# Kernel tuning notes

Hardware: AMD Instinct MI355X
Metric: run time of the kernel (lower is better)

The kernel has to match this reference:

```python
import jax, jax.numpy as jnp
import numpy as np

B, S, D, L = 4, 4096, 2048, 4
QH, KVH, WINDOW = 16, 4, 512
HD = D // QH
G = QH // KVH
CAPF = 0.25
EPS = float(jnp.finfo(jnp.float32).eps)  # torch RMSNorm default eps for fp32


def setup_inputs() -> dict:
    key = jax.random.key(0)
    ks = jax.random.split(key, 8)
    s = 0.02
    return {
        "x": jax.random.normal(ks[0], (B, S, D), jnp.float32),
        "router_w": jax.random.normal(ks[1], (1, D), jnp.float32) * s,
        "norm1_w": jnp.ones((L, D), jnp.float32),
        "norm2_w": jnp.ones((L, D), jnp.float32),
        "qkv_w": jax.random.normal(ks[2], (L, (QH + 2 * KVH) * HD, D), jnp.float32) * s,
        "proj_w": jax.random.normal(ks[3], (L, D, D), jnp.float32) * s,
        "fc1_w": jax.random.normal(ks[4], (L, 2 * D, D), jnp.float32) * s,
        "fc2_w": jax.random.normal(ks[5], (L, D, D), jnp.float32) * s,
    }


def rmsnorm(x, w):
    return x * jax.lax.rsqrt(jnp.mean(x * x, -1, keepdims=True) + EPS) * w


def gqa(x, qkv_w, proj_w):
    # x: [B, C, D]; causal sliding-window attention with ALiBi (flash_attn semantics)
    b, c, _ = x.shape
    qkv = x @ qkv_w.T
    q = qkv[..., : QH * HD].reshape(b, c, KVH, G, HD)
    k = qkv[..., QH * HD:(QH + KVH) * HD].reshape(b, c, KVH, HD)
    v = qkv[..., (QH + KVH) * HD:].reshape(b, c, KVH, HD)
    scale = 1.0 / np.sqrt(HD)
    scores = jnp.einsum('bqkgd,bskd->bkgqs', q, k) * scale  # [B,KVH,G,C,C]
    i = jnp.arange(c)[:, None]
    j = jnp.arange(c)[None, :]
    diff = (i - j).astype(jnp.float32)
    mask = (diff >= 0) & (diff <= WINDOW)  # causal + left window
    slopes = jnp.exp2(-((jnp.arange(QH, dtype=jnp.float32) + 1.0) * 8.0 / QH))
    slopes = slopes.reshape(KVH, G, 1, 1)  # q head h = kvh*G + g ordering
    scores = jnp.where(mask, scores - slopes * diff, -jnp.inf)
    p = jax.nn.softmax(scores, axis=-1)
    att = jnp.einsum('bkgqs,bskd->bqkgd', p, v).reshape(b, c, QH * HD)
    return att @ proj_w.T


def swiglu(x, fc1_w, fc2_w):
    h = x @ fc1_w.T
    a, gate = jnp.split(h, 2, axis=-1)
    return (jax.nn.silu(gate) * a) @ fc2_w.T


def reference(x, router_w, norm1_w, norm2_w, qkv_w, proj_w, fc1_w, fc2_w):
    b, s, d = x.shape
    rw = jax.nn.sigmoid(x @ router_w.T)  # [B, S, 1]
    cap = int(s * CAPF)  # training path: capacity = int(seq_len * capacity_factor)
    rws = rw[..., 0]
    _, top_idx = jax.lax.top_k(rws, cap)            # unsorted-by-position top-k
    idx_sorted = jnp.sort(top_idx, axis=1)          # restore sequence order
    order = jnp.argsort(top_idx, axis=1)
    # faithful to source: gathers router_weights at the sort-order permutation
    # indices (values in [0, cap)), exactly as torch.gather(router_weights, 1, router_top_order)
    top_w = jnp.take_along_axis(rws, order, axis=1)[..., None]  # [B, cap, 1]
    lat = jnp.take_along_axis(x, idx_sorted[..., None], axis=1)  # [B, cap, D]
    for l in range(L):
        lat = lat + gqa(rmsnorm(lat, norm1_w[l]), qkv_w[l], proj_w[l])
        lat = lat + swiglu(rmsnorm(lat, norm2_w[l]), fc1_w[l], fc2_w[l])
    lat = lat * top_w
    bidx = jnp.arange(b)[:, None]
    pred = jnp.zeros_like(x).at[bidx, idx_sorted].set(lat)
    decisions = jnp.zeros_like(rw).at[bidx, idx_sorted].set(1.0)
    return pred, rw, decisions
```

## Files before the change

### kernel.cpp

```cpp
#include <hip/hip_runtime.h>
#include <hip/hip_bf16.h>

constexpr int NB = 4;
constexpr int SEQ = 4096;
constexpr int DIM = 2048;
constexpr int NLAYER = 4;
constexpr int NQH = 16;
constexpr int NKVH = 4;
constexpr int WIN = 512;
constexpr int HDIM = 128;
constexpr int CAPN = 1024;
constexpr int MTOK = NB * CAPN;
constexpr int QKVN = (NQH + 2 * NKVH) * HDIM;
constexpr int VOFF = DIM + NKVH * HDIM;
constexpr float EPSF = 1.1920928955078125e-07f;

typedef __hip_bfloat16 bf16;
typedef __bf16 b16x8 __attribute__((ext_vector_type(8)));
typedef __bf16 b16x4 __attribute__((ext_vector_type(4)));
typedef float f32x4 __attribute__((ext_vector_type(4)));

#define MFMA16(a, b, c) __builtin_amdgcn_mfma_f32_16x16x32_bf16((a), (b), (c), 0, 0, 0)

__device__ __forceinline__ void gload_lds16(const void* g, void* l) {
  __builtin_amdgcn_global_load_lds((__attribute__((address_space(1))) void*)(void*)g,
                                   (__attribute__((address_space(3))) void*)l, 16, 0, 0);
}

__global__ __launch_bounds__(256) void cast_kernel(const float* __restrict__ in,
                                                   bf16* __restrict__ out, int n) {
  int i = (blockIdx.x * 256 + threadIdx.x) * 4;
  if (i >= n) return;
  float4 v = *(const float4*)(in + i);
  b16x4 o;
  o[0] = (__bf16)v.x; o[1] = (__bf16)v.y; o[2] = (__bf16)v.z; o[3] = (__bf16)v.w;
  *(b16x4*)((__bf16*)out + i) = o;
}

__global__ __launch_bounds__(256) void router_kernel(const float* __restrict__ x,
                                                     const float* __restrict__ rwt,
                                                     float* __restrict__ rw_out) {
  int tok = blockIdx.x * 4 + (threadIdx.x >> 6);
  int l = threadIdx.x & 63;
  const float* xr = x + (size_t)tok * DIM;
  float s = 0.f;
  for (int c = l; c < DIM; c += 64) s += xr[c] * rwt[c];
  for (int off = 32; off; off >>= 1) s += __shfl_down(s, off);
  if (l == 0) rw_out[tok] = 1.f / (1.f + expf(-s));
}

__global__ __launch_bounds__(256) void rankcnt_kernel(const float* __restrict__ rw,
                                                      int* __restrict__ rank) {
  int blk = blockIdx.x;
  int ic = blk & 15, jc = (blk >> 4) & 15, b = blk >> 8;
  __shared__ float4 svi[64];
  int t = threadIdx.x;
  if (t < 64) svi[t] = ((const float4*)(rw + (size_t)b * SEQ + ic * 256))[t];
  __syncthreads();
  int j = jc * 256 + t;
  float vj = rw[(size_t)b * SEQ + j];
  int r = 0;
#pragma unroll 16
  for (int q = 0; q < 64; ++q) {
    float4 v = svi[q];
    int i = ic * 256 + q * 4;
    r += (v.x > vj || (v.x == vj && (i + 0) < j)) ? 1 : 0;
    r += (v.y > vj || (v.y == vj && (i + 1) < j)) ? 1 : 0;
    r += (v.z > vj || (v.z == vj && (i + 2) < j)) ? 1 : 0;
    r += (v.w > vj || (v.w == vj && (i + 3) < j)) ? 1 : 0;
  }
  atomicAdd(&rank[b * SEQ + j], r);
}

__global__ __launch_bounds__(1024) void select_kernel(const int* __restrict__ rank,
                                                      const float* __restrict__ rw,
                                                      int* __restrict__ idxs,
                                                      float* __restrict__ topw,
                                                      float* __restrict__ dec) {
  int b = blockIdx.x;
  int t = threadIdx.x;
  __shared__ int sr[SEQ];
  __shared__ int scnt[1024];
  for (int i = t; i < SEQ; i += 1024) sr[i] = rank[b * SEQ + i];
  __syncthreads();
  for (int i = t; i < SEQ; i += 1024) dec[(size_t)b * SEQ + i] = (sr[i] < CAPN) ? 1.0f : 0.0f;
  int c = 0;
#pragma unroll
  for (int k = 0; k < 4; ++k) c += (sr[t * 4 + k] < CAPN) ? 1 : 0;
  scnt[t] = c;
  __syncthreads();
  for (int off = 1; off < 1024; off <<= 1) {
    int v = scnt[t];
    int vm = (t >= off) ? scnt[t - off] : 0;
    __syncthreads();
    scnt[t] = v + vm;
    __syncthreads();
  }
  int pos = scnt[t] - c;
  for (int k = 0; k < 4; ++k) {
    int j = t * 4 + k;
    int r = sr[j];
    if (r < CAPN) {
      idxs[b * CAPN + pos] = j;
      topw[b * CAPN + pos] = rw[(size_t)b * SEQ + r];
      pos++;
    }
  }
}

__global__ __launch_bounds__(256) void gather_kernel(const float* __restrict__ x,
                                                     const int* __restrict__ idxs,
                                                     float* __restrict__ lat) {
  int tok = blockIdx.x;
  int b = tok >> 10, i = tok & 1023;
  int src = idxs[b * CAPN + i];
  const float4* sp = (const float4*)(x + ((size_t)b * SEQ + src) * DIM);
  float4* dp = (float4*)(lat + (size_t)tok * DIM);
  int t = threadIdx.x;
  dp[t] = sp[t];
  dp[t + 256] = sp[t + 256];
}

__global__ __launch_bounds__(256) void rmsnorm_kernel(const float* __restrict__ in,
                                                      const float* __restrict__ w,
                                                      bf16* __restrict__ out) {
  int row = blockIdx.x;
  int t = threadIdx.x;
  const float4* sp = (const float4*)(in + (size_t)row * DIM);
  float4 v0 = sp[t], v1 = sp[t + 256];
  float ss = v0.x * v0.x + v0.y * v0.y + v0.z * v0.z + v0.w * v0.w +
             v1.x * v1.x + v1.y * v1.y + v1.z * v1.z + v1.w * v1.w;
  for (int off = 32; off; off >>= 1) ss += __shfl_down(ss, off);
  __shared__ float red[4];
  if ((t & 63) == 0) red[t >> 6] = ss;
  __syncthreads();
  float total = red[0] + red[1] + red[2] + red[3];
  float sc = rsqrtf(total * (1.0f / DIM) + EPSF);
  const float4* wp = (const float4*)w;
  float4 w0 = wp[t], w1 = wp[t + 256];
  __bf16* op = (__bf16*)out + (size_t)row * DIM;
  b16x4 o0, o1;
  o0[0] = (__bf16)(v0.x * w0.x * sc); o0[1] = (__bf16)(v0.y * w0.y * sc);
  o0[2] = (__bf16)(v0.z * w0.z * sc); o0[3] = (__bf16)(v0.w * w0.w * sc);
  o1[0] = (__bf16)(v1.x * w1.x * sc); o1[1] = (__bf16)(v1.y * w1.y * sc);
  o1[2] = (__bf16)(v1.z * w1.z * sc); o1[3] = (__bf16)(v1.w * w1.w * sc);
  *(b16x4*)(op + t * 4) = o0;
  *(b16x4*)(op + 1024 + t * 4) = o1;
}


template <int ROWS>
__device__ __forceinline__ void stage_tile(const bf16* gbase, int ldk, int kt,
                                           bf16* lbuf, int tid) {
#pragma unroll
  for (int i = 0; i < ROWS / 128; ++i) {
    int q = i * 8192 + tid * 16;
    int row = q >> 6;
    int ce = ((tid & 3) ^ ((row >> 1) & 3)) << 3;
    gload_lds16((const __bf16*)gbase + (size_t)row * ldk + kt * 32 + ce,
                (char*)lbuf + q);
  }
}

__device__ __forceinline__ b16x8 frag_ld(const bf16* buf, int row, int hi) {
  int ce = (hi ^ ((row >> 1) & 3)) << 3;
  return *(const b16x8*)((const __bf16*)buf + row * 32 + ce);
}

template <int MR, bool ADD, bool OUTBF>
__global__ __launch_bounds__(512, 2) void gemm256(const bf16* __restrict__ A,
                                                  const bf16* __restrict__ Bw,
                                                  float* __restrict__ Cf,
                                                  bf16* __restrict__ Cb,
                                                  bf16* __restrict__ vTout,
                                                  int N, int K, int nbn) {
  constexpr int BM = MR * 32;
  constexpr int PH = MR / 4;
  __shared__ __align__(16) bf16 sA[4][BM * 32];
  __shared__ __align__(16) bf16 sB[4][256 * 32];
  const int tid = threadIdx.x;
  const int w = tid >> 6, l = tid & 63;
  const int lo = l & 15, hi = l >> 4;
  const int wm = w >> 2, wn = w & 3;
  const int nwg = gridDim.x;
  int bid = blockIdx.x;
  bid = (bid & 7) * (nwg >> 3) + (bid >> 3);
  const int bm = bid / nbn, bn = bid % nbn;
  const bf16* Ab = A + (size_t)bm * BM * K;
  const bf16* Bb = Bw + (size_t)bn * 256 * K;
  const int nt = K >> 5;

  f32x4 acc[MR][4];
#pragma unroll
  for (int i = 0; i < MR; ++i)
#pragma unroll
    for (int j = 0; j < 4; ++j) acc[i][j] = f32x4{0.f, 0.f, 0.f, 0.f};

  for (int tt = 0; tt < 3; ++tt) {
    stage_tile<BM>(Ab, K, tt, sA[tt], tid);
    stage_tile<256>(Bb, K, tt, sB[tt], tid);
  }
  if constexpr (MR == 8) asm volatile("s_waitcnt vmcnt(8)" ::: "memory");
  else                   asm volatile("s_waitcnt vmcnt(6)" ::: "memory");
  __builtin_amdgcn_sched_barrier(0);
  __builtin_amdgcn_s_barrier();

  for (int t = 0; t < nt; ++t) {
    const bf16* bufA = sA[t & 3];
    const bf16* bufB = sB[t & 3];
    b16x8 bfr[4];
#pragma unroll
    for (int p = 0; p < PH; ++p) {
      b16x8 af[4];
#pragma unroll
      for (int mi = 0; mi < 4; ++mi)
        af[mi] = frag_ld(bufA, wm * (MR * 16) + p * 64 + mi * 16 + lo, hi);
      if (p == 0) {
#pragma unroll
        for (int ni = 0; ni < 4; ++ni)
          bfr[ni] = frag_ld(bufB, wn * 64 + ni * 16 + lo, hi);
      }
      if (t + 3 < nt) {
        if (p == 0) stage_tile<BM>(Ab, K, t + 3, sA[(t + 3) & 3], tid);
        if (p == PH - 1) stage_tile<256>(Bb, K, t + 3, sB[(t + 3) & 3], tid);
      }
      __builtin_amdgcn_s_barrier();
      __builtin_amdgcn_s_setprio(1);
#pragma unroll
      for (int mi = 0; mi < 4; ++mi)
#pragma unroll
        for (int ni = 0; ni < 4; ++ni)
          acc[p * 4 + mi][ni] = MFMA16(af[mi], bfr[ni], acc[p * 4 + mi][ni]);
      __builtin_amdgcn_s_setprio(0);
      if (p == PH - 1) {
        if (t + 3 < nt) {
          if constexpr (MR == 8) asm volatile("s_waitcnt vmcnt(8)" ::: "memory");
          else                   asm volatile("s_waitcnt vmcnt(6)" ::: "memory");
        } else if (t + 2 < nt) {
          if constexpr (MR == 8) asm volatile("s_waitcnt vmcnt(4)" ::: "memory");
          else                   asm volatile("s_waitcnt vmcnt(3)" ::: "memory");
        } else if (t + 1 < nt) {
          asm volatile("s_waitcnt vmcnt(0)" ::: "memory");
        }
        __builtin_amdgcn_sched_barrier(0);
      }
      __builtin_amdgcn_s_barrier();
    }
  }

#pragma unroll
  for (int mi = 0; mi < MR; ++mi) {
    int row0 = bm * BM + wm * (MR * 16) + mi * 16 + hi * 4;
#pragma unroll
    for (int ni = 0; ni < 4; ++ni) {
      int col = bn * 256 + wn * 64 + ni * 16 + lo;
#pragma unroll
      for (int r = 0; r < 4; ++r) {
        size_t idx = (size_t)(row0 + r) * N + col;
        float v = acc[mi][ni][r];
        if constexpr (ADD) v += Cf[idx];
        if constexpr (OUTBF) {
          bf16 bv = __float2bfloat16(v);
          Cb[idx] = bv;
          if (vTout != nullptr && col >= VOFF) {
            int cc = col - VOFF;
            int kvh = cc >> 7, d = cc & 127;
            int row = row0 + r;
            int bb = row >> 10, tk = row & 1023;
            vTout[((size_t)(bb * NKVH + kvh) * HDIM + d) * CAPN + tk] = bv;
          }
        } else {
          Cf[idx] = v;
        }
      }
    }
  }
}

__global__ __launch_bounds__(256) void attn_kernel(const bf16* __restrict__ qkvb,
                                                   const bf16* __restrict__ vT,
                                                   bf16* __restrict__ attb) {
  const int blk = blockIdx.x;
  const int qc = blk & 31;
  const int kvh = (blk >> 5) & 3;
  const int b = blk >> 7;
  const int w = threadIdx.x >> 6, l = threadIdx.x & 63;
  const int lo = l & 15, hi = l >> 4;
  const int h = kvh * 4 + w;
  const float slope = exp2f(-0.5f * (float)(h + 1));
  const float scale = 0.08838834764831845f;
  __shared__ __align__(16) bf16 p_lds[4][2][16 * 32];
  const __bf16* qp = (const __bf16*)qkvb;
  const __bf16* vtp = (const __bf16*)vT + (size_t)(b * NKVH + kvh) * HDIM * CAPN;
  const size_t tb = (size_t)b * CAPN;
  const int i0b = qc * 32;

  b16x8 aq[2][4];
#pragma unroll
  for (int qt = 0; qt < 2; ++qt) {
    const __bf16* qrow = qp + (tb + i0b + qt * 16 + lo) * QKVN + h * HDIM + hi * 8;
#pragma unroll
    for (int c = 0; c < 4; ++c) aq[qt][c] = *(const b16x8*)(qrow + c * 32);
  }

  f32x4 acc[2][8];
#pragma unroll
  for (int qt = 0; qt < 2; ++qt)
#pragma unroll
    for (int d = 0; d < 8; ++d) acc[qt][d] = f32x4{0.f, 0.f, 0.f, 0.f};
  float mrow[2][4], ssum[2][4];
#pragma unroll
  for (int qt = 0; qt < 2; ++qt)
#pragma unroll
    for (int r = 0; r < 4; ++r) { mrow[qt][r] = -1e30f; ssum[qt][r] = 0.f; }

  int jlo = i0b - WIN;
  if (jlo < 0) jlo = 0;
  jlo &= ~31;
  for (int j0 = jlo; j0 <= i0b; j0 += 32) {
    b16x8 kf[2][4];
#pragma unroll
    for (int jt = 0; jt < 2; ++jt) {
      const __bf16* krow = qp + (tb + j0 + jt * 16 + lo) * QKVN + DIM + kvh * HDIM + hi * 8;
#pragma unroll
      for (int c = 0; c < 4; ++c) kf[jt][c] = *(const b16x8*)(krow + c * 32);
    }
    f32x4 s[2][2];
#pragma unroll
    for (int qt = 0; qt < 2; ++qt)
#pragma unroll
      for (int jt = 0; jt < 2; ++jt) {
        s[qt][jt] = f32x4{0.f, 0.f, 0.f, 0.f};
#pragma unroll
        for (int c = 0; c < 4; ++c) s[qt][jt] = MFMA16(aq[qt][c], kf[jt][c], s[qt][jt]);
      }
#pragma unroll
    for (int qt = 0; qt < 2; ++qt) {
#pragma unroll
      for (int r = 0; r < 4; ++r) {
        const int i = i0b + qt * 16 + hi * 4 + r;
        float d0f = (float)(i - (j0 + lo));
        float d1f = (float)(i - (j0 + 16 + lo));
        float v0 = (d0f >= 0.f && d0f <= 512.f) ? (s[qt][0][r] * scale - slope * d0f) : -1e30f;
        float v1 = (d1f >= 0.f && d1f <= 512.f) ? (s[qt][1][r] * scale - slope * d1f) : -1e30f;
        float tm = fmaxf(v0, v1);
#pragma unroll
        for (int off = 1; off < 16; off <<= 1) tm = fmaxf(tm, __shfl_xor(tm, off));
        float mnew = fmaxf(mrow[qt][r], tm);
        float e0 = (v0 > -1e29f) ? __expf(v0 - mnew) : 0.f;
        float e1 = (v1 > -1e29f) ? __expf(v1 - mnew) : 0.f;
        float rs = e0 + e1;
#pragma unroll
        for (int off = 1; off < 16; off <<= 1) rs += __shfl_xor(rs, off);
        float corr = (mrow[qt][r] > -1e29f) ? __expf(mrow[qt][r] - mnew) : 0.f;
        ssum[qt][r] = ssum[qt][r] * corr + rs;
        mrow[qt][r] = mnew;
#pragma unroll
        for (int d = 0; d < 8; ++d) acc[qt][d][r] *= corr;
        p_lds[w][qt][(hi * 4 + r) * 32 + lo] = __float2bfloat16(e0);
        p_lds[w][qt][(hi * 4 + r) * 32 + 16 + lo] = __float2bfloat16(e1);
      }
    }
    b16x8 pa[2];
    pa[0] = *(const b16x8*)((const __bf16*)p_lds[w][0] + lo * 32 + hi * 8);
    pa[1] = *(const b16x8*)((const __bf16*)p_lds[w][1] + lo * 32 + hi * 8);
#pragma unroll
    for (int dh = 0; dh < 2; ++dh) {
      b16x8 bv[4];
#pragma unroll
      for (int dd = 0; dd < 4; ++dd) {
        int d = dh * 4 + dd;
        bv[dd] = *(const b16x8*)(vtp + (size_t)(d * 16 + lo) * CAPN + j0 + hi * 8);
      }
#pragma unroll
      for (int qt = 0; qt < 2; ++qt)
#pragma unroll
        for (int dd = 0; dd < 4; ++dd)
          acc[qt][dh * 4 + dd] = MFMA16(pa[qt], bv[dd], acc[qt][dh * 4 + dd]);
    }
  }
#pragma unroll
  for (int qt = 0; qt < 2; ++qt)
#pragma unroll
    for (int d = 0; d < 8; ++d)
#pragma unroll
      for (int r = 0; r < 4; ++r) {
        int row = i0b + qt * 16 + hi * 4 + r;
        attb[(tb + row) * DIM + h * HDIM + d * 16 + lo] =
            __float2bfloat16(acc[qt][d][r] / ssum[qt][r]);
      }
}

__global__ __launch_bounds__(256) void swiglu_kernel(const bf16* __restrict__ hb,
                                                     bf16* __restrict__ out) {
  int row = blockIdx.x;
  int c = threadIdx.x * 8;
  const __bf16* hp = (const __bf16*)hb + (size_t)row * (2 * DIM);
  b16x8 a8 = *(const b16x8*)(hp + c);
  b16x8 g8 = *(const b16x8*)(hp + DIM + c);
  b16x8 o;
#pragma unroll
  for (int i = 0; i < 8; ++i) {
    float a = (float)a8[i], g = (float)g8[i];
    float sg = g / (1.f + __expf(-g));
    o[i] = (__bf16)(sg * a);
  }
  *(b16x8*)((__bf16*)out + (size_t)row * DIM + c) = o;
}

__global__ __launch_bounds__(256) void scatter_kernel(const float* __restrict__ lat,
                                                      const int* __restrict__ idxs,
                                                      const float* __restrict__ topw,
                                                      float* __restrict__ pred) {
  int tok = blockIdx.x;
  int b = tok >> 10, i = tok & 1023;
  int dst = idxs[b * CAPN + i];
  float wv = topw[b * CAPN + i];
  const float4* sp = (const float4*)(lat + (size_t)tok * DIM);
  float4* dp = (float4*)(pred + ((size_t)b * SEQ + dst) * DIM);
  int t = threadIdx.x;
  float4 v = sp[t];
  v.x *= wv; v.y *= wv; v.z *= wv; v.w *= wv;
  dp[t] = v;
  v = sp[t + 256];
  v.x *= wv; v.y *= wv; v.z *= wv; v.w *= wv;
  dp[t + 256] = v;
}

extern "C" void kernel_launch(void* const* d_in, const int* in_sizes, int n_in,
                              void* d_out, int out_size, void* d_ws, size_t ws_size,
                              hipStream_t stream) {
  const float* x        = (const float*)d_in[0];
  const float* router_w = (const float*)d_in[1];
  const float* norm1_w  = (const float*)d_in[2];
  const float* norm2_w  = (const float*)d_in[3];
  const float* qkv_w    = (const float*)d_in[4];
  const float* proj_w   = (const float*)d_in[5];
  const float* fc1_w    = (const float*)d_in[6];
  const float* fc2_w    = (const float*)d_in[7];

  float* pred   = (float*)d_out;
  float* rw_out = pred + (size_t)NB * SEQ * DIM;
  float* dec    = rw_out + (size_t)NB * SEQ;

  char* ws = (char*)d_ws;
  float* lat  = (float*)ws; ws += (size_t)MTOK * DIM * 4;
  bf16* xn    = (bf16*)ws;  ws += (size_t)MTOK * DIM * 2;
  bf16* qkvb  = (bf16*)ws;  ws += (size_t)MTOK * QKVN * 2;
  bf16* attb  = (bf16*)ws;  ws += (size_t)MTOK * DIM * 2;
  int* rank   = (int*)ws;   ws += (size_t)NB * SEQ * 4;
  int* idxs   = (int*)ws;   ws += (size_t)NB * CAPN * 4;
  float* topw = (float*)ws; ws += (size_t)NB * CAPN * 4;

  char* sp = (char*)pred;
  bf16* hb = (bf16*)sp; sp += (size_t)MTOK * (2 * DIM) * 2;
  bf16* wq = (bf16*)sp; sp += (size_t)QKVN * DIM * 2;
  bf16* wp = (bf16*)sp; sp += (size_t)DIM * DIM * 2;
  bf16* w1 = (bf16*)sp; sp += (size_t)(2 * DIM) * DIM * 2;
  bf16* w2 = (bf16*)sp; sp += (size_t)DIM * DIM * 2;
  bf16* vT = (bf16*)sp; sp += (size_t)NB * NKVH * HDIM * CAPN * 2;

  router_kernel<<<NB * SEQ / 4, 256, 0, stream>>>(x, router_w, rw_out);
  hipMemsetAsync(rank, 0, (size_t)NB * SEQ * 4, stream);
  rankcnt_kernel<<<NB * 256, 256, 0, stream>>>(rw_out, rank);
  select_kernel<<<NB, 1024, 0, stream>>>(rank, rw_out, idxs, topw, dec);
  gather_kernel<<<MTOK, 256, 0, stream>>>(x, idxs, lat);

  for (int l = 0; l < NLAYER; ++l) {
    cast_kernel<<<(QKVN * DIM) / 1024, 256, 0, stream>>>(qkv_w + (size_t)l * QKVN * DIM, wq, QKVN * DIM);
    cast_kernel<<<(DIM * DIM) / 1024, 256, 0, stream>>>(proj_w + (size_t)l * DIM * DIM, wp, DIM * DIM);
    cast_kernel<<<(2 * DIM * DIM) / 1024, 256, 0, stream>>>(fc1_w + (size_t)l * 2 * DIM * DIM, w1, 2 * DIM * DIM);
    cast_kernel<<<(DIM * DIM) / 1024, 256, 0, stream>>>(fc2_w + (size_t)l * DIM * DIM, w2, DIM * DIM);

    rmsnorm_kernel<<<MTOK, 256, 0, stream>>>(lat, norm1_w + (size_t)l * DIM, xn);
    gemm256<8, false, true><<<(MTOK / 256) * (QKVN / 256), 512, 0, stream>>>(
        xn, wq, nullptr, qkvb, vT, QKVN, DIM, QKVN / 256);
    attn_kernel<<<NB * NKVH * 32, 256, 0, stream>>>(qkvb, vT, attb);
    gemm256<4, true, false><<<(MTOK / 128) * (DIM / 256), 512, 0, stream>>>(
        attb, wp, lat, nullptr, nullptr, DIM, DIM, DIM / 256);

    rmsnorm_kernel<<<MTOK, 256, 0, stream>>>(lat, norm2_w + (size_t)l * DIM, xn);
    gemm256<8, false, true><<<(MTOK / 256) * (2 * DIM / 256), 512, 0, stream>>>(
        xn, w1, nullptr, hb, nullptr, 2 * DIM, DIM, 2 * DIM / 256);
    swiglu_kernel<<<MTOK, 256, 0, stream>>>(hb, xn);
    gemm256<4, true, false><<<(MTOK / 128) * (DIM / 256), 512, 0, stream>>>(
        xn, w2, lat, nullptr, nullptr, DIM, DIM, DIM / 256);
  }

  hipMemsetAsync(pred, 0, (size_t)NB * SEQ * DIM * 4, stream);
  scatter_kernel<<<MTOK, 256, 0, stream>>>(lat, idxs, topw, pred);
}
```

Before: 1.704 ms.

## Add 8-wave ping-pong GEMM with BK=64 tiles for QKV and FC1 projections

Introduces a new 256x256 GEMM kernel that uses 64-wide K tiles with XOR-swizzled LDS, double buffering, and a fine-grained schedule interleaving half-tile global loads with quadrant MFMA blocks separated by barriers and priority hints. It also remaps block IDs across eight groups to improve L2 locality. The QKV and FC1 GEMMs switch to it, and the old kernel drops its V-transpose epilogue. The aim is better overlap of memory loads with MFMA work. The cost is a larger LDS footprint (128 KB) and many barriers, which could hurt occupancy or add stalls.

Result: no change. 1.675 ms (-1.7%).

```diff
diff --git a/kernel.cpp b/kernel.cpp
--- a/kernel.cpp
+++ b/kernel.cpp
@@ -149,6 +149,150 @@
 }
 
 
+__device__ __forceinline__ void stage_half(const bf16* g, int K, int kt,
+                                           bf16* tilebase, int h, int tid) {
+#pragma unroll
+  for (int j = 0; j < 2; ++j) {
+    int q = h * 16384 + j * 8192 + tid * 16;
+    int row = q >> 7;
+    int sc = ((tid & 7) ^ (row & 7)) << 3;
+    gload_lds16((const __bf16*)g + (size_t)row * K + kt * 64 + sc,
+                (char*)tilebase + q);
+  }
+}
+
+__device__ __forceinline__ b16x8 frag8(const bf16* buf, int row, int ks, int hi) {
+  int co = (ks * 32 + hi * 8) ^ ((row & 7) << 3);
+  return *(const b16x8*)((const __bf16*)buf + row * 64 + co);
+}
+
+template <bool VT>
+__global__ __launch_bounds__(512) void gemm8p(const bf16* __restrict__ A,
+                                              const bf16* __restrict__ Bw,
+                                              bf16* __restrict__ Cb,
+                                              bf16* __restrict__ vTout,
+                                              int N, int K, int nbn) {
+  __shared__ __align__(16) bf16 sA[2][256 * 64];
+  __shared__ __align__(16) bf16 sB[2][256 * 64];
+  const int tid = threadIdx.x;
+  const int w = tid >> 6, l = tid & 63;
+  const int lo = l & 15, hi = l >> 4;
+  const int wm = w >> 2, wn = w & 3;
+  const int nwg = gridDim.x;
+  int bid = blockIdx.x;
+  bid = (bid & 7) * (nwg >> 3) + (bid >> 3);
+  const int bm = bid / nbn, bn = bid % nbn;
+  const bf16* Ab = A + (size_t)bm * 256 * K;
+  const bf16* Bb = Bw + (size_t)bn * 256 * K;
+  const int nt = K >> 6;
+  const int niter = nt >> 1;
+
+  f32x4 acc[8][4];
+#pragma unroll
+  for (int i = 0; i < 8; ++i)
+#pragma unroll
+    for (int j = 0; j < 4; ++j) acc[i][j] = f32x4{0.f, 0.f, 0.f, 0.f};
+
+#define LDA_Q(BUF, QM)                                                      \
+  do {                                                                      \
+    _Pragma("unroll") for (int mi = 0; mi < 4; ++mi)                        \
+        _Pragma("unroll") for (int ks = 0; ks < 2; ++ks)                    \
+            af[mi][ks] = frag8((BUF), wm * 128 + (QM)*64 + mi * 16 + lo, ks, hi); \
+  } while (0)
+#define LDB_Q(BUF, QN, DST)                                                 \
+  do {                                                                      \
+    _Pragma("unroll") for (int ni = 0; ni < 2; ++ni)                        \
+        _Pragma("unroll") for (int ks = 0; ks < 2; ++ks)                    \
+            DST[ni][ks] = frag8((BUF), wn * 64 + (QN)*32 + ni * 16 + lo, ks, hi); \
+  } while (0)
+#define MM_Q(QM, QN, BFR)                                                   \
+  do {                                                                      \
+    __builtin_amdgcn_s_setprio(1);                                          \
+    _Pragma("unroll") for (int ks = 0; ks < 2; ++ks)                        \
+        _Pragma("unroll") for (int mi = 0; mi < 4; ++mi)                    \
+            _Pragma("unroll") for (int ni = 0; ni < 2; ++ni)                \
+                acc[(QM)*4 + mi][(QN)*2 + ni] =                             \
+                    MFMA16(af[mi][ks], BFR[ni][ks], acc[(QM)*4 + mi][(QN)*2 + ni]); \
+    __builtin_amdgcn_s_setprio(0);                                          \
+  } while (0)
+#define BAR() __builtin_amdgcn_s_barrier()
+
+  stage_half(Ab, K, 0, sA[0], 0, tid);
+  stage_half(Ab, K, 0, sA[0], 1, tid);
+  stage_half(Bb, K, 0, sB[0], 0, tid);
+  stage_half(Bb, K, 0, sB[0], 1, tid);
+  stage_half(Bb, K, 1, sB[1], 0, tid);
+  stage_half(Bb, K, 1, sB[1], 1, tid);
+  stage_half(Ab, K, 1, sA[1], 0, tid);
+  asm volatile("s_waitcnt vmcnt(6)" ::: "memory");
+  __builtin_amdgcn_sched_barrier(0);
+  BAR();
+
+  for (int i = 0; i < niter; ++i) {
+    const int t0 = 2 * i;
+    const bool s2 = (t0 + 2) < nt;
+    b16x8 af[4][2], bf0[2][2], bf1[2][2];
+    LDA_Q(sA[0], 0); LDB_Q(sB[0], 0, bf0);
+    stage_half(Ab, K, t0 + 1, sA[1], 1, tid);
+    BAR(); MM_Q(0, 0, bf0); BAR();
+    LDB_Q(sB[0], 1, bf1);
+    BAR(); MM_Q(0, 1, bf1); BAR();
+    LDA_Q(sA[0], 1);
+    if (s2) stage_half(Bb, K, t0 + 2, sB[0], 0, tid);
+    BAR(); MM_Q(1, 0, bf0); BAR();
+    if (s2) stage_half(Bb, K, t0 + 2, sB[0], 1, tid);
+    BAR(); MM_Q(1, 1, bf1);
+    if (s2) asm volatile("s_waitcnt vmcnt(4)" ::: "memory");
+    else    asm volatile("s_waitcnt vmcnt(0)" ::: "memory");
+    __builtin_amdgcn_sched_barrier(0);
+    BAR();
+    LDA_Q(sA[1], 0); LDB_Q(sB[1], 0, bf0);
+    if (s2) stage_half(Ab, K, t0 + 2, sA[0], 0, tid);
+    BAR(); MM_Q(0, 0, bf0); BAR();
+    LDB_Q(sB[1], 1, bf1);
+    if (s2) stage_half(Ab, K, t0 + 2, sA[0], 1, tid);
+    BAR(); MM_Q(0, 1, bf1); BAR();
+    LDA_Q(sA[1], 1);
+    if (s2) { stage_half(Bb, K, t0 + 3, sB[1], 0, tid);
+              stage_half(Bb, K, t0 + 3, sB[1], 1, tid); }
+    BAR(); MM_Q(1, 0, bf0); BAR();
+    if (s2) stage_half(Ab, K, t0 + 3, sA[1], 0, tid);
+    BAR(); MM_Q(1, 1, bf1);
+    if (s2) {
+      asm volatile("s_waitcnt vmcnt(6)" ::: "memory");
+      __builtin_amdgcn_sched_barrier(0);
+    }
+    BAR();
+  }
+#undef LDA_Q
+#undef LDB_Q
+#undef MM_Q
+#undef BAR
+
+#pragma unroll
+  for (int fi = 0; fi < 8; ++fi) {
+    int row0 = bm * 256 + wm * 128 + fi * 16 + hi * 4;
+#pragma unroll
+    for (int fj = 0; fj < 4; ++fj) {
+      int col = bn * 256 + wn * 64 + fj * 16 + lo;
+#pragma unroll
+      for (int r = 0; r < 4; ++r) {
+        bf16 bv = __float2bfloat16(acc[fi][fj][r]);
+        Cb[(size_t)(row0 + r) * N + col] = bv;
+        if constexpr (VT) {
+          if (col >= VOFF) {
+            int cc = col - VOFF;
+            int kvh = cc >> 7, d = cc & 127;
+            int row = row0 + r;
+            int bb = row >> 10, tk = row & 1023;
+            vTout[((size_t)(bb * NKVH + kvh) * HDIM + d) * CAPN + tk] = bv;
+          }
+        }
+      }
+    }
+  }
+}
+
 template <int ROWS>
 __device__ __forceinline__ void stage_tile(const bf16* gbase, int ldk, int kt,
                                            bf16* lbuf, int tid) {
@@ -260,15 +404,7 @@
         float v = acc[mi][ni][r];
         if constexpr (ADD) v += Cf[idx];
         if constexpr (OUTBF) {
-          bf16 bv = __float2bfloat16(v);
-          Cb[idx] = bv;
-          if (vTout != nullptr && col >= VOFF) {
-            int cc = col - VOFF;
-            int kvh = cc >> 7, d = cc & 127;
-            int row = row0 + r;
-            int bb = row >> 10, tk = row & 1023;
-            vTout[((size_t)(bb * NKVH + kvh) * HDIM + d) * CAPN + tk] = bv;
-          }
+          Cb[idx] = __float2bfloat16(v);
         } else {
           Cf[idx] = v;
         }
@@ -473,15 +609,15 @@
     cast_kernel<<<(DIM * DIM) / 1024, 256, 0, stream>>>(fc2_w + (size_t)l * DIM * DIM, w2, DIM * DIM);
 
     rmsnorm_kernel<<<MTOK, 256, 0, stream>>>(lat, norm1_w + (size_t)l * DIM, xn);
-    gemm256<8, false, true><<<(MTOK / 256) * (QKVN / 256), 512, 0, stream>>>(
-        xn, wq, nullptr, qkvb, vT, QKVN, DIM, QKVN / 256);
+    gemm8p<true><<<(MTOK / 256) * (QKVN / 256), 512, 0, stream>>>(
+        xn, wq, qkvb, vT, QKVN, DIM, QKVN / 256);
     attn_kernel<<<NB * NKVH * 32, 256, 0, stream>>>(qkvb, vT, attb);
     gemm256<4, true, false><<<(MTOK / 128) * (DIM / 256), 512, 0, stream>>>(
         attb, wp, lat, nullptr, nullptr, DIM, DIM, DIM / 256);
 
     rmsnorm_kernel<<<MTOK, 256, 0, stream>>>(lat, norm2_w + (size_t)l * DIM, xn);
-    gemm256<8, false, true><<<(MTOK / 256) * (2 * DIM / 256), 512, 0, stream>>>(
-        xn, w1, nullptr, hb, nullptr, 2 * DIM, DIM, 2 * DIM / 256);
+    gemm8p<false><<<(MTOK / 256) * (2 * DIM / 256), 512, 0, stream>>>(
+        xn, w1, hb, nullptr, 2 * DIM, DIM, 2 * DIM / 256);
     swiglu_kernel<<<MTOK, 256, 0, stream>>>(hb, xn);
     gemm256<4, true, false><<<(MTOK / 128) * (DIM / 256), 512, 0, stream>>>(
         xn, w2, lat, nullptr, nullptr, DIM, DIM, DIM / 256);
```

## Replace pipelined GEMM with simpler 128x128 kernel and fuse SwiGLU into fc1

Applied to the files above, without the earlier changes.

Swaps the 256-wide, 4-stage software-pipelined GEMM for a 128x128 tile GEMM with a single LDS buffer, a BK of 64 and synchronous staging at 256 threads per block. The fc1 weight rows are interleaved in 16-row chunks of value and gate during the cast, so each output tile holds matching value and gate columns and SwiGLU is applied in the GEMM epilogue. This removes the separate swiglu kernel and the round trip of the 2*DIM hidden buffer. The trade-off is losing multi-stage prefetch and overlap of loads with MFMA, which may expose memory latency.

After: 1.499 ms. 1.14x faster.

```diff
diff --git a/kernel.cpp b/kernel.cpp
--- a/kernel.cpp
+++ b/kernel.cpp
@@ -37,6 +37,23 @@
   *(b16x4*)((__bf16*)out + i) = o;
 }
 
+__global__ __launch_bounds__(256) void cast_fc1_kernel(const float* __restrict__ in,
+                                                       bf16* __restrict__ out) {
+  int p = blockIdx.x;
+  int chunk = p >> 5, w = p & 31;
+  int L = (w < 16) ? (chunk * 16 + w) : (DIM + chunk * 16 + (w - 16));
+  const float4* spv = (const float4*)(in + (size_t)L * DIM);
+  __bf16* op = (__bf16*)out + (size_t)p * DIM;
+  int t = threadIdx.x;
+#pragma unroll
+  for (int j = 0; j < 2; ++j) {
+    float4 v = spv[t + j * 256];
+    b16x4 o;
+    o[0] = (__bf16)v.x; o[1] = (__bf16)v.y; o[2] = (__bf16)v.z; o[3] = (__bf16)v.w;
+    *(b16x4*)(op + (t + j * 256) * 4) = o;
+  }
+}
+
 __global__ __launch_bounds__(256) void router_kernel(const float* __restrict__ x,
                                                      const float* __restrict__ rwt,
                                                      float* __restrict__ rw_out) {
@@ -114,11 +131,11 @@
   int tok = blockIdx.x;
   int b = tok >> 10, i = tok & 1023;
   int src = idxs[b * CAPN + i];
-  const float4* sp = (const float4*)(x + ((size_t)b * SEQ + src) * DIM);
+  const float4* spv = (const float4*)(x + ((size_t)b * SEQ + src) * DIM);
   float4* dp = (float4*)(lat + (size_t)tok * DIM);
   int t = threadIdx.x;
-  dp[t] = sp[t];
-  dp[t + 256] = sp[t + 256];
+  dp[t] = spv[t];
+  dp[t + 256] = spv[t + 256];
 }
 
 __global__ __launch_bounds__(256) void rmsnorm_kernel(const float* __restrict__ in,
@@ -126,8 +143,8 @@
                                                       bf16* __restrict__ out) {
   int row = blockIdx.x;
   int t = threadIdx.x;
-  const float4* sp = (const float4*)(in + (size_t)row * DIM);
-  float4 v0 = sp[t], v1 = sp[t + 256];
+  const float4* spv = (const float4*)(in + (size_t)row * DIM);
+  float4 v0 = spv[t], v1 = spv[t + 256];
   float ss = v0.x * v0.x + v0.y * v0.y + v0.z * v0.z + v0.w * v0.w +
              v1.x * v1.x + v1.y * v1.y + v1.z * v1.z + v1.w * v1.w;
   for (int off = 32; off; off >>= 1) ss += __shfl_down(ss, off);
@@ -149,128 +166,110 @@
 }
 
 
-template <int ROWS>
-__device__ __forceinline__ void stage_tile(const bf16* gbase, int ldk, int kt,
-                                           bf16* lbuf, int tid) {
-#pragma unroll
-  for (int i = 0; i < ROWS / 128; ++i) {
-    int q = i * 8192 + tid * 16;
-    int row = q >> 6;
-    int ce = ((tid & 3) ^ ((row >> 1) & 3)) << 3;
-    gload_lds16((const __bf16*)gbase + (size_t)row * ldk + kt * 32 + ce,
-                (char*)lbuf + q);
-  }
-}
-
-__device__ __forceinline__ b16x8 frag_ld(const bf16* buf, int row, int hi) {
-  int ce = (hi ^ ((row >> 1) & 3)) << 3;
-  return *(const b16x8*)((const __bf16*)buf + row * 32 + ce);
-}
-
-template <int MR, bool ADD, bool OUTBF>
-__global__ __launch_bounds__(512, 2) void gemm256(const bf16* __restrict__ A,
-                                                  const bf16* __restrict__ Bw,
-                                                  float* __restrict__ Cf,
-                                                  bf16* __restrict__ Cb,
-                                                  bf16* __restrict__ vTout,
-                                                  int N, int K, int nbn) {
-  constexpr int BM = MR * 32;
-  constexpr int PH = MR / 4;
-  __shared__ __align__(16) bf16 sA[4][BM * 32];
-  __shared__ __align__(16) bf16 sB[4][256 * 32];
+__device__ __forceinline__ void stage97(const bf16* g, int K, int kt,
+                                        bf16* tile, int tid) {
+#pragma unroll
+  for (int j = 0; j < 4; ++j) {
+    int q = j * 4096 + tid * 16;
+    int row = q >> 7;
+    int sc = ((tid & 7) ^ (row & 7)) << 3;
+    gload_lds16((const __bf16*)g + (size_t)row * K + kt * 64 + sc,
+                (char*)tile + q);
+  }
+}
+
+__device__ __forceinline__ b16x8 frag97(const bf16* buf, int row, int ks, int hi) {
+  int co = (ks * 32 + hi * 8) ^ ((row & 7) << 3);
+  return *(const b16x8*)((const __bf16*)buf + row * 64 + co);
+}
+
+template <int MODE>
+__global__ __launch_bounds__(256, 3) void gemm97(const bf16* __restrict__ A,
+                                                 const bf16* __restrict__ Bw,
+                                                 float* __restrict__ Cf,
+                                                 bf16* __restrict__ Cb,
+                                                 bf16* __restrict__ vTout,
+                                                 int N, int K, int nbn) {
+  __shared__ __align__(16) bf16 sA[128 * 64];
+  __shared__ __align__(16) bf16 sB[128 * 64];
   const int tid = threadIdx.x;
   const int w = tid >> 6, l = tid & 63;
   const int lo = l & 15, hi = l >> 4;
-  const int wm = w >> 2, wn = w & 3;
+  const int wr = w >> 1, wc = w & 1;
   const int nwg = gridDim.x;
   int bid = blockIdx.x;
   bid = (bid & 7) * (nwg >> 3) + (bid >> 3);
   const int bm = bid / nbn, bn = bid % nbn;
-  const bf16* Ab = A + (size_t)bm * BM * K;
-  const bf16* Bb = Bw + (size_t)bn * 256 * K;
-  const int nt = K >> 5;
-
-  f32x4 acc[MR][4];
-#pragma unroll
-  for (int i = 0; i < MR; ++i)
+  const bf16* Ab = A + (size_t)bm * 128 * K;
+  const bf16* Bb = Bw + (size_t)bn * 128 * K;
+  const int nt = K >> 6;
+
+  f32x4 acc[4][4];
+#pragma unroll
+  for (int i = 0; i < 4; ++i)
 #pragma unroll
     for (int j = 0; j < 4; ++j) acc[i][j] = f32x4{0.f, 0.f, 0.f, 0.f};
 
-  for (int tt = 0; tt < 3; ++tt) {
-    stage_tile<BM>(Ab, K, tt, sA[tt], tid);
-    stage_tile<256>(Bb, K, tt, sB[tt], tid);
-  }
-  if constexpr (MR == 8) asm volatile("s_waitcnt vmcnt(8)" ::: "memory");
-  else                   asm volatile("s_waitcnt vmcnt(6)" ::: "memory");
-  __builtin_amdgcn_sched_barrier(0);
-  __builtin_amdgcn_s_barrier();
-
   for (int t = 0; t < nt; ++t) {
-    const bf16* bufA = sA[t & 3];
-    const bf16* bufB = sB[t & 3];
-    b16x8 bfr[4];
-#pragma unroll
-    for (int p = 0; p < PH; ++p) {
-      b16x8 af[4];
+    stage97(Ab, K, t, sA, tid);
+    stage97(Bb, K, t, sB, tid);
+    __syncthreads();
+#pragma unroll
+    for (int ks = 0; ks < 2; ++ks) {
+      b16x8 af[4], bfm[4];
 #pragma unroll
       for (int mi = 0; mi < 4; ++mi)
-        af[mi] = frag_ld(bufA, wm * (MR * 16) + p * 64 + mi * 16 + lo, hi);
-      if (p == 0) {
+        af[mi] = frag97(sA, wr * 64 + mi * 16 + lo, ks, hi);
+#pragma unroll
+      for (int ni = 0; ni < 4; ++ni)
+        bfm[ni] = frag97(sB, wc * 64 + ni * 16 + lo, ks, hi);
+#pragma unroll
+      for (int mi = 0; mi < 4; ++mi)
 #pragma unroll
         for (int ni = 0; ni < 4; ++ni)
-          bfr[ni] = frag_ld(bufB, wn * 64 + ni * 16 + lo, hi);
-      }
-      if (t + 3 < nt) {
-        if (p == 0) stage_tile<BM>(Ab, K, t + 3, sA[(t + 3) & 3], tid);
-        if (p == PH - 1) stage_tile<256>(Bb, K, t + 3, sB[(t + 3) & 3], tid);
-      }
-      __builtin_amdgcn_s_barrier();
-      __builtin_amdgcn_s_setprio(1);
-#pragma unroll
-      for (int mi = 0; mi < 4; ++mi)
-#pragma unroll
-        for (int ni = 0; ni < 4; ++ni)
-          acc[p * 4 + mi][ni] = MFMA16(af[mi], bfr[ni], acc[p * 4 + mi][ni]);
-      __builtin_amdgcn_s_setprio(0);
-      if (p == PH - 1) {
-        if (t + 3 < nt) {
-          if constexpr (MR == 8) asm volatile("s_waitcnt vmcnt(8)" ::: "memory");
-          else                   asm volatile("s_waitcnt vmcnt(6)" ::: "memory");
-        } else if (t + 2 < nt) {
-          if constexpr (MR == 8) asm volatile("s_waitcnt vmcnt(4)" ::: "memory");
-          else                   asm volatile("s_waitcnt vmcnt(3)" ::: "memory");
-        } else if (t + 1 < nt) {
-          asm volatile("s_waitcnt vmcnt(0)" ::: "memory");
+          acc[mi][ni] = MFMA16(af[mi], bfm[ni], acc[mi][ni]);
+    }
+    __syncthreads();
+  }
+
+#pragma unroll
+  for (int mi = 0; mi < 4; ++mi) {
+    int row0 = bm * 128 + wr * 64 + mi * 16 + hi * 4;
+    if constexpr (MODE == 2) {
+#pragma unroll
+      for (int j2 = 0; j2 < 2; ++j2) {
+        int colL = bn * 64 + wc * 32 + j2 * 16 + lo;
+#pragma unroll
+        for (int r = 0; r < 4; ++r) {
+          float a = acc[mi][2 * j2][r];
+          float g = acc[mi][2 * j2 + 1][r];
+          float s = g / (1.f + __expf(-g));
+          Cb[(size_t)(row0 + r) * DIM + colL] = __float2bfloat16(a * s);
         }
-        __builtin_amdgcn_sched_barrier(0);
-      }
-      __builtin_amdgcn_s_barrier();
-    }
-  }
-
-#pragma unroll
-  for (int mi = 0; mi < MR; ++mi) {
-    int row0 = bm * BM + wm * (MR * 16) + mi * 16 + hi * 4;
-#pragma unroll
-    for (int ni = 0; ni < 4; ++ni) {
-      int col = bn * 256 + wn * 64 + ni * 16 + lo;
-#pragma unroll
-      for (int r = 0; r < 4; ++r) {
-        size_t idx = (size_t)(row0 + r) * N + col;
-        float v = acc[mi][ni][r];
-        if constexpr (ADD) v += Cf[idx];
-        if constexpr (OUTBF) {
-          bf16 bv = __float2bfloat16(v);
-          Cb[idx] = bv;
-          if (vTout != nullptr && col >= VOFF) {
-            int cc = col - VOFF;
-            int kvh = cc >> 7, d = cc & 127;
-            int row = row0 + r;
-            int bb = row >> 10, tk = row & 1023;
-            vTout[((size_t)(bb * NKVH + kvh) * HDIM + d) * CAPN + tk] = bv;
+      }
+    } else {
+#pragma unroll
+      for (int ni = 0; ni < 4; ++ni) {
+        int col = bn * 128 + wc * 64 + ni * 16 + lo;
+#pragma unroll
+        for (int r = 0; r < 4; ++r) {
+          size_t idx = (size_t)(row0 + r) * N + col;
+          float v = acc[mi][ni][r];
+          if constexpr (MODE == 3) {
+            Cf[idx] += v;
+          } else {
+            bf16 bv = __float2bfloat16(v);
+            Cb[idx] = bv;
+            if constexpr (MODE == 1) {
+              if (col >= VOFF) {
+                int cc = col - VOFF;
+                int kvh = cc >> 7, d = cc & 127;
+                int row = row0 + r;
+                int bb = row >> 10, tk = row & 1023;
+                vTout[((size_t)(bb * NKVH + kvh) * HDIM + d) * CAPN + tk] = bv;
+              }
+            }
           }
-        } else {
-          Cf[idx] = v;
         }
       }
     }
@@ -391,23 +390,6 @@
       }
 }
 
-__global__ __launch_bounds__(256) void swiglu_kernel(const bf16* __restrict__ hb,
-                                                     bf16* __restrict__ out) {
-  int row = blockIdx.x;
-  int c = threadIdx.x * 8;
-  const __bf16* hp = (const __bf16*)hb + (size_t)row * (2 * DIM);
-  b16x8 a8 = *(const b16x8*)(hp + c);
-  b16x8 g8 = *(const b16x8*)(hp + DIM + c);
-  b16x8 o;
-#pragma unroll
-  for (int i = 0; i < 8; ++i) {
-    float a = (float)a8[i], g = (float)g8[i];
-    float sg = g / (1.f + __expf(-g));
-    o[i] = (__bf16)(sg * a);
-  }
-  *(b16x8*)((__bf16*)out + (size_t)row * DIM + c) = o;
-}
-
 __global__ __launch_bounds__(256) void scatter_kernel(const float* __restrict__ lat,
                                                       const int* __restrict__ idxs,
                                                       const float* __restrict__ topw,
@@ -416,13 +398,13 @@
   int b = tok >> 10, i = tok & 1023;
   int dst = idxs[b * CAPN + i];
   float wv = topw[b * CAPN + i];
-  const float4* sp = (const float4*)(lat + (size_t)tok * DIM);
+  const float4* spv = (const float4*)(lat + (size_t)tok * DIM);
   float4* dp = (float4*)(pred + ((size_t)b * SEQ + dst) * DIM);
   int t = threadIdx.x;
-  float4 v = sp[t];
+  float4 v = spv[t];
   v.x *= wv; v.y *= wv; v.z *= wv; v.w *= wv;
   dp[t] = v;
-  v = sp[t + 256];
+  v = spv[t + 256];
   v.x *= wv; v.y *= wv; v.z *= wv; v.w *= wv;
   dp[t + 256] = v;
 }
@@ -453,7 +435,7 @@
   float* topw = (float*)ws; ws += (size_t)NB * CAPN * 4;
 
   char* sp = (char*)pred;
-  bf16* hb = (bf16*)sp; sp += (size_t)MTOK * (2 * DIM) * 2;
+  sp += (size_t)MTOK * (2 * DIM) * 2;
   bf16* wq = (bf16*)sp; sp += (size_t)QKVN * DIM * 2;
   bf16* wp = (bf16*)sp; sp += (size_t)DIM * DIM * 2;
   bf16* w1 = (bf16*)sp; sp += (size_t)(2 * DIM) * DIM * 2;
@@ -469,22 +451,21 @@
   for (int l = 0; l < NLAYER; ++l) {
     cast_kernel<<<(QKVN * DIM) / 1024, 256, 0, stream>>>(qkv_w + (size_t)l * QKVN * DIM, wq, QKVN * DIM);
     cast_kernel<<<(DIM * DIM) / 1024, 256, 0, stream>>>(proj_w + (size_t)l * DIM * DIM, wp, DIM * DIM);
-    cast_kernel<<<(2 * DIM * DIM) / 1024, 256, 0, stream>>>(fc1_w + (size_t)l * 2 * DIM * DIM, w1, 2 * DIM * DIM);
+    cast_fc1_kernel<<<2 * DIM, 256, 0, stream>>>(fc1_w + (size_t)l * 2 * DIM * DIM, w1);
     cast_kernel<<<(DIM * DIM) / 1024, 256, 0, stream>>>(fc2_w + (size_t)l * DIM * DIM, w2, DIM * DIM);
 
     rmsnorm_kernel<<<MTOK, 256, 0, stream>>>(lat, norm1_w + (size_t)l * DIM, xn);
-    gemm256<8, false, true><<<(MTOK / 256) * (QKVN / 256), 512, 0, stream>>>(
-        xn, wq, nullptr, qkvb, vT, QKVN, DIM, QKVN / 256);
+    gemm97<1><<<(MTOK / 128) * (QKVN / 128), 256, 0, stream>>>(
+        xn, wq, nullptr, qkvb, vT, QKVN, DIM, QKVN / 128);
     attn_kernel<<<NB * NKVH * 32, 256, 0, stream>>>(qkvb, vT, attb);
-    gemm256<4, true, false><<<(MTOK / 128) * (DIM / 256), 512, 0, stream>>>(
-        attb, wp, lat, nullptr, nullptr, DIM, DIM, DIM / 256);
+    gemm97<3><<<(MTOK / 128) * (DIM / 128), 256, 0, stream>>>(
+        attb, wp, lat, nullptr, nullptr, DIM, DIM, DIM / 128);
 
     rmsnorm_kernel<<<MTOK, 256, 0, stream>>>(lat, norm2_w + (size_t)l * DIM, xn);
-    gemm256<8, false, true><<<(MTOK / 256) * (2 * DIM / 256), 512, 0, stream>>>(
-        xn, w1, nullptr, hb, nullptr, 2 * DIM, DIM, 2 * DIM / 256);
-    swiglu_kernel<<<MTOK, 256, 0, stream>>>(hb, xn);
-    gemm256<4, true, false><<<(MTOK / 128) * (DIM / 256), 512, 0, stream>>>(
-        xn, w2, lat, nullptr, nullptr, DIM, DIM, DIM / 256);
+    gemm97<2><<<(MTOK / 128) * (2 * DIM / 128), 256, 0, stream>>>(
+        xn, w1, nullptr, attb, nullptr, 2 * DIM, DIM, 2 * DIM / 128);
+    gemm97<3><<<(MTOK / 128) * (DIM / 128), 256, 0, stream>>>(
+        attb, w2, lat, nullptr, nullptr, DIM, DIM, DIM / 128);
   }
 
   hipMemsetAsync(pred, 0, (size_t)NB * SEQ * DIM * 4, stream);
```
